# Kernel tuning notes

Hardware: AMD Instinct MI355X
Metric: run time of the kernel (lower is better)

## Reference

```python
import jax, jax.numpy as jnp
import numpy as np

NUM_CLASSES = 6

def _weight_matrix(num_classes, weight_type='quadratic'):
    i = jnp.arange(num_classes, dtype=jnp.float32)
    d = jnp.abs(i[:, None] - i[None, :])
    if weight_type == 'linear':
        return d
    elif weight_type == 'quadratic':
        return d ** 2
    else:
        raise ValueError("weight_type must be 'linear' or 'quadratic'")

def setup_inputs() -> dict:
    key = jax.random.key(0)
    k1, k2 = jax.random.split(key)
    N = 4_000_000
    y_pred = jax.random.normal(k1, (N, NUM_CLASSES), dtype=jnp.float32)
    y_true = jax.random.randint(k2, (N,), 0, NUM_CLASSES, dtype=jnp.int64)
    return {"y_pred": y_pred, "y_true": y_true}

def reference(y_pred, y_true):
    C = NUM_CLASSES
    t = y_true.reshape(-1).astype(jnp.int32)
    probs = jax.nn.softmax(y_pred, axis=1)
    p = jnp.argmax(probs, axis=1).astype(jnp.int32)
    # histograms over classes (equivalent to torch.histc with bins=C, min=0, max=C-1)
    hist_true = jnp.bincount(t, length=C).astype(jnp.float32)
    hist_pred = jnp.bincount(p, length=C).astype(jnp.float32)
    # confusion matrix in one fused scatter-add pass (replaces the Python loop)
    flat = t * C + p  # [N]
    confusion = jnp.bincount(flat, length=C * C).astype(jnp.float32).reshape(C, C)
    confusion = confusion / confusion.sum()
    expected = jnp.outer(hist_true, hist_pred)
    expected = expected / expected.sum()
    W = _weight_matrix(C, 'quadratic')
    kappa = 1.0 - (W * confusion).sum() / (W * expected).sum()
    return kappa
```

## Files before the change

kernel.cpp:

```cpp
#include <hip/hip_runtime.h>


#define NC 6
#define NBINS 36
#define GRID 1024
#define SEGS 16
#define FIN_THREADS (NBINS * SEGS)

__global__ void kappa_count_kernel(const float4* __restrict__ yp4,
                                   const int2* __restrict__ yt2,
                                   const float* __restrict__ yp,
                                   const int* __restrict__ yt,
                                   unsigned int* __restrict__ gconf,
                                   int npairs, int N) {
    __shared__ unsigned int sconf[NBINS];
    const int tid = threadIdx.x;
    if (tid < NBINS) sconf[tid] = 0u;
    __syncthreads();

    const int stride = gridDim.x * blockDim.x;
    for (int i = blockIdx.x * blockDim.x + tid; i < npairs; i += stride) {
        const float4 a = yp4[3 * i];
        const float4 b = yp4[3 * i + 1];
        const float4 c = yp4[3 * i + 2];
        const int2 t = yt2[i];

        float m = a.x; int p = 0;
        if (a.y > m) { m = a.y; p = 1; }
        if (a.z > m) { m = a.z; p = 2; }
        if (a.w > m) { m = a.w; p = 3; }
        if (b.x > m) { m = b.x; p = 4; }
        if (b.y > m) { m = b.y; p = 5; }
        atomicAdd(&sconf[t.x * NC + p], 1u);

        m = b.z; p = 0;
        if (b.w > m) { m = b.w; p = 1; }
        if (c.x > m) { m = c.x; p = 2; }
        if (c.y > m) { m = c.y; p = 3; }
        if (c.z > m) { m = c.z; p = 4; }
        if (c.w > m) { m = c.w; p = 5; }
        atomicAdd(&sconf[t.y * NC + p], 1u);
    }

    if ((N & 1) && blockIdx.x == 0 && tid == 0) {
        const int r = N - 1;
        float m = yp[r * NC]; int p = 0;
        #pragma unroll
        for (int j = 1; j < NC; ++j) {
            const float v = yp[r * NC + j];
            if (v > m) { m = v; p = j; }
        }
        atomicAdd(&sconf[yt[r] * NC + p], 1u);
    }

    __syncthreads();
    if (tid < NBINS) gconf[blockIdx.x * NBINS + tid] = sconf[tid];
}

__global__ void kappa_final_kernel(const unsigned int* __restrict__ gconf,
                                   float* __restrict__ out, long long N) {
    __shared__ unsigned int part[SEGS][NBINS];
    __shared__ unsigned int conf_s[NBINS];
    const int tid = threadIdx.x;
    if (tid < FIN_THREADS) {
        const int bin = tid % NBINS;
        const int seg = tid / NBINS;
        unsigned int s = 0;
        const int b0 = seg * (GRID / SEGS);
        #pragma unroll 8
        for (int b = b0; b < b0 + GRID / SEGS; ++b) s += gconf[b * NBINS + bin];
        part[seg][bin] = s;
    }
    __syncthreads();
    if (tid < NBINS) {
        unsigned int tot = 0;
        #pragma unroll
        for (int s2 = 0; s2 < SEGS; ++s2) tot += part[s2][tid];
        conf_s[tid] = tot;
    }
    __syncthreads();
    if (tid == 0) {
        long long conf[NBINS], ht[NC], hp[NC];
        #pragma unroll
        for (int i = 0; i < NC; ++i) { ht[i] = 0; hp[i] = 0; }
        #pragma unroll
        for (int k = 0; k < NBINS; ++k) conf[k] = (long long)conf_s[k];

        long long num = 0;
        #pragma unroll
        for (int i = 0; i < NC; ++i)
            #pragma unroll
            for (int j = 0; j < NC; ++j) {
                const long long w = (long long)(i - j) * (i - j);
                num += w * conf[i * NC + j];
                ht[i] += conf[i * NC + j];
                hp[j] += conf[i * NC + j];
            }
        long long den = 0;
        #pragma unroll
        for (int i = 0; i < NC; ++i)
            #pragma unroll
            for (int j = 0; j < NC; ++j)
                den += (long long)(i - j) * (i - j) * ht[i] * hp[j];

        out[0] = (float)(1.0 - ((double)num * (double)N) / (double)den);
    }
}

extern "C" void kernel_launch(void* const* d_in, const int* in_sizes, int n_in,
                              void* d_out, int out_size, void* d_ws, size_t ws_size,
                              hipStream_t stream) {
    const float* yp = (const float*)d_in[0];
    const int* yt = (const int*)d_in[1];
    const int N = in_sizes[1];
    unsigned int* gconf = (unsigned int*)d_ws;

    const int npairs = N / 2;
    kappa_count_kernel<<<GRID, 256, 0, stream>>>(
        (const float4*)yp, (const int2*)yt, yp, yt, gconf, npairs, N);
    kappa_final_kernel<<<1, FIN_THREADS, 0, stream>>>(gconf, (float*)d_out,
                                                      (long long)N);
}
```

Baseline: 153.3 us.

## Fuse count and finalize kernels via last-block atomic reduction with replicated bins

Merges the counting and final reduction kernels into one launch: each block adds its 36 bins into one of 8 replicated global bin sets with atomics, and the last block, found through an atomic counter, sums the replicas and computes kappa. Shared histograms are split into 4 copies, one per 64-thread wavefront, to reduce LDS atomic contention. The grid is doubled to 2048 blocks. This removes the second launch and the 1024-row partial-sum pass, at the cost of a memset per call and global atomic traffic.

Measured after the change: 244.4 us. 1.59x slower.

```diff
diff --git a/kernel.cpp b/kernel.cpp
--- a/kernel.cpp
+++ b/kernel.cpp
@@ -3,21 +3,25 @@
 
 #define NC 6
 #define NBINS 36
-#define GRID 1024
-#define SEGS 16
-#define FIN_THREADS (NBINS * SEGS)
+#define NREP 8
+#define GRID 2048
+#define BLOCK 256
 
-__global__ void kappa_count_kernel(const float4* __restrict__ yp4,
-                                   const int2* __restrict__ yt2,
-                                   const float* __restrict__ yp,
-                                   const int* __restrict__ yt,
-                                   unsigned int* __restrict__ gconf,
-                                   int npairs, int N) {
-    __shared__ unsigned int sconf[NBINS];
+__global__ __launch_bounds__(BLOCK) void kappa_fused(
+    const float4* __restrict__ yp4, const int2* __restrict__ yt2,
+    const float* __restrict__ yp, const int* __restrict__ yt,
+    unsigned int* __restrict__ gbins,
+    unsigned int* __restrict__ counter,
+    float* __restrict__ out, int npairs, int N) {
+    __shared__ unsigned int sconf[4][NBINS];
+    __shared__ unsigned int stot[NBINS];
+    __shared__ unsigned int last_flag;
     const int tid = threadIdx.x;
-    if (tid < NBINS) sconf[tid] = 0u;
+    if (tid < 4 * NBINS) ((unsigned int*)sconf)[tid] = 0u;
+    if (tid == 0) last_flag = 0u;
     __syncthreads();
 
+    unsigned int* __restrict__ my = sconf[tid >> 6];
     const int stride = gridDim.x * blockDim.x;
     for (int i = blockIdx.x * blockDim.x + tid; i < npairs; i += stride) {
         const float4 a = yp4[3 * i];
@@ -31,7 +35,7 @@
         if (a.w > m) { m = a.w; p = 3; }
         if (b.x > m) { m = b.x; p = 4; }
         if (b.y > m) { m = b.y; p = 5; }
-        atomicAdd(&sconf[t.x * NC + p], 1u);
+        atomicAdd(&my[t.x * NC + p], 1u);
 
         m = b.z; p = 0;
         if (b.w > m) { m = b.w; p = 1; }
@@ -39,7 +43,7 @@
         if (c.y > m) { m = c.y; p = 3; }
         if (c.z > m) { m = c.z; p = 4; }
         if (c.w > m) { m = c.w; p = 5; }
-        atomicAdd(&sconf[t.y * NC + p], 1u);
+        atomicAdd(&my[t.y * NC + p], 1u);
     }
 
     if ((N & 1) && blockIdx.x == 0 && tid == 0) {
@@ -50,33 +54,31 @@
             const float v = yp[r * NC + j];
             if (v > m) { m = v; p = j; }
         }
-        atomicAdd(&sconf[yt[r] * NC + p], 1u);
-    }
-
-    __syncthreads();
-    if (tid < NBINS) gconf[blockIdx.x * NBINS + tid] = sconf[tid];
-}
-
-__global__ void kappa_final_kernel(const unsigned int* __restrict__ gconf,
-                                   float* __restrict__ out, long long N) {
-    __shared__ unsigned int part[SEGS][NBINS];
-    __shared__ unsigned int conf_s[NBINS];
-    const int tid = threadIdx.x;
-    if (tid < FIN_THREADS) {
-        const int bin = tid % NBINS;
-        const int seg = tid / NBINS;
-        unsigned int s = 0;
-        const int b0 = seg * (GRID / SEGS);
-        #pragma unroll 8
-        for (int b = b0; b < b0 + GRID / SEGS; ++b) s += gconf[b * NBINS + bin];
-        part[seg][bin] = s;
+        atomicAdd(&my[yt[r] * NC + p], 1u);
     }
     __syncthreads();
+
     if (tid < NBINS) {
-        unsigned int tot = 0;
+        const unsigned int s =
+            sconf[0][tid] + sconf[1][tid] + sconf[2][tid] + sconf[3][tid];
+        if (s) atomicAdd(&gbins[(blockIdx.x & (NREP - 1)) * NBINS + tid], s);
+    }
+    __syncthreads();
+
+    if (tid == 0) {
+        __threadfence();
+        if (atomicAdd(counter, 1u) == (unsigned int)(GRID - 1)) last_flag = 1u;
+    }
+    __syncthreads();
+    if (!last_flag) return;
+
+    if (tid < NBINS) {
+        unsigned int s = 0;
         #pragma unroll
-        for (int s2 = 0; s2 < SEGS; ++s2) tot += part[s2][tid];
-        conf_s[tid] = tot;
+        for (int r = 0; r < NREP; ++r)
+            s += __hip_atomic_load(&gbins[r * NBINS + tid], __ATOMIC_RELAXED,
+                                   __HIP_MEMORY_SCOPE_AGENT);
+        stot[tid] = s;
     }
     __syncthreads();
     if (tid == 0) {
@@ -84,7 +86,7 @@
         #pragma unroll
         for (int i = 0; i < NC; ++i) { ht[i] = 0; hp[i] = 0; }
         #pragma unroll
-        for (int k = 0; k < NBINS; ++k) conf[k] = (long long)conf_s[k];
+        for (int k = 0; k < NBINS; ++k) conf[k] = (long long)stot[k];
 
         long long num = 0;
         #pragma unroll
@@ -103,7 +105,7 @@
             for (int j = 0; j < NC; ++j)
                 den += (long long)(i - j) * (i - j) * ht[i] * hp[j];
 
-        out[0] = (float)(1.0 - ((double)num * (double)N) / (double)den);
+        out[0] = (float)(1.0 - ((double)num * (double)(long long)N) / (double)den);
     }
 }
 
@@ -113,11 +115,13 @@
     const float* yp = (const float*)d_in[0];
     const int* yt = (const int*)d_in[1];
     const int N = in_sizes[1];
-    unsigned int* gconf = (unsigned int*)d_ws;
+    unsigned int* gbins = (unsigned int*)d_ws;
+    unsigned int* counter = gbins + NREP * NBINS;
+
+    hipMemsetAsync(d_ws, 0, (NREP * NBINS + 1) * sizeof(unsigned int), stream);
 
     const int npairs = N / 2;
-    kappa_count_kernel<<<GRID, 256, 0, stream>>>(
-        (const float4*)yp, (const int2*)yt, yp, yt, gconf, npairs, N);
-    kappa_final_kernel<<<1, FIN_THREADS, 0, stream>>>(gconf, (float*)d_out,
-                                                      (long long)N);
+    kappa_fused<<<GRID, BLOCK, 0, stream>>>(
+        (const float4*)yp, (const int2*)yt, yp, yt, gbins, counter,
+        (float*)d_out, npairs, N);
 }
```

## Stage loads through LDS per wave and privatize histograms per wave

Applied to the files above, without the earlier changes.

Each wave now loads a 64-pair chunk of predictions with contiguous, coalesced float4 reads into shared memory, then reads back each lane's 6-float rows. The confusion histogram is privatized per wave in shared memory and summed at block end, so fewer threads contend on the same 36 LDS atomic counters. The launch changes to 512 blocks of 1024 threads, and a tail path handles pairs left over after the last full chunk. It relies on wave-level lockstep with only a block fence between the LDS write and read, and it uses more shared memory per block.

Measured after the change: 155.6 us. About the same (+1.5%).

```diff
diff --git a/kernel.cpp b/kernel.cpp
--- a/kernel.cpp
+++ b/kernel.cpp
@@ -3,27 +3,42 @@
 
 #define NC 6
 #define NBINS 36
-#define GRID 1024
+#define BLOCK 1024
+#define NWAVES (BLOCK / 64)
+#define GRID 512
+#define CHUNK 64
 #define SEGS 16
 #define FIN_THREADS (NBINS * SEGS)
 
-__global__ void kappa_count_kernel(const float4* __restrict__ yp4,
-                                   const int2* __restrict__ yt2,
-                                   const float* __restrict__ yp,
-                                   const int* __restrict__ yt,
-                                   unsigned int* __restrict__ gconf,
-                                   int npairs, int N) {
-    __shared__ unsigned int sconf[NBINS];
+__global__ __launch_bounds__(BLOCK, 8) void kappa_count(
+    const float4* __restrict__ yp4, const int2* __restrict__ yt2,
+    const float* __restrict__ yp, const int* __restrict__ yt,
+    unsigned int* __restrict__ gconf, int npairs, int N) {
+    __shared__ float4 stage[NWAVES][3 * CHUNK];
+    __shared__ unsigned int sconf[NWAVES][NBINS];
     const int tid = threadIdx.x;
-    if (tid < NBINS) sconf[tid] = 0u;
+    const int w = tid >> 6;
+    const int L = tid & 63;
+    if (tid < NWAVES * NBINS) ((unsigned int*)sconf)[tid] = 0u;
     __syncthreads();
 
-    const int stride = gridDim.x * blockDim.x;
-    for (int i = blockIdx.x * blockDim.x + tid; i < npairs; i += stride) {
-        const float4 a = yp4[3 * i];
-        const float4 b = yp4[3 * i + 1];
-        const float4 c = yp4[3 * i + 2];
-        const int2 t = yt2[i];
+    unsigned int* my = sconf[w];
+    float4* st = stage[w];
+
+    const int nchunks = npairs / CHUNK;
+    const int gwaves = GRID * NWAVES;
+    for (int c = blockIdx.x * NWAVES + w; c < nchunks; c += gwaves) {
+        const float4 g0 = yp4[c * 3 * CHUNK + L];
+        const float4 g1 = yp4[c * 3 * CHUNK + 64 + L];
+        const float4 g2 = yp4[c * 3 * CHUNK + 128 + L];
+        const int2 t = yt2[c * CHUNK + L];
+        st[L] = g0;
+        st[64 + L] = g1;
+        st[128 + L] = g2;
+        __threadfence_block();
+        const float4 a = st[3 * L];
+        const float4 b = st[3 * L + 1];
+        const float4 d = st[3 * L + 2];
 
         float m = a.x; int p = 0;
         if (a.y > m) { m = a.y; p = 1; }
@@ -31,15 +46,38 @@
         if (a.w > m) { m = a.w; p = 3; }
         if (b.x > m) { m = b.x; p = 4; }
         if (b.y > m) { m = b.y; p = 5; }
-        atomicAdd(&sconf[t.x * NC + p], 1u);
+        atomicAdd(&my[t.x * NC + p], 1u);
 
         m = b.z; p = 0;
         if (b.w > m) { m = b.w; p = 1; }
-        if (c.x > m) { m = c.x; p = 2; }
-        if (c.y > m) { m = c.y; p = 3; }
-        if (c.z > m) { m = c.z; p = 4; }
-        if (c.w > m) { m = c.w; p = 5; }
-        atomicAdd(&sconf[t.y * NC + p], 1u);
+        if (d.x > m) { m = d.x; p = 2; }
+        if (d.y > m) { m = d.y; p = 3; }
+        if (d.z > m) { m = d.z; p = 4; }
+        if (d.w > m) { m = d.w; p = 5; }
+        atomicAdd(&my[t.y * NC + p], 1u);
+    }
+
+    const int rem0 = nchunks * CHUNK;
+    if (blockIdx.x == 0 && tid < npairs - rem0) {
+        const int i = rem0 + tid;
+        const float4 a = yp4[3 * i];
+        const float4 b = yp4[3 * i + 1];
+        const float4 d = yp4[3 * i + 2];
+        const int2 t = yt2[i];
+        float m = a.x; int p = 0;
+        if (a.y > m) { m = a.y; p = 1; }
+        if (a.z > m) { m = a.z; p = 2; }
+        if (a.w > m) { m = a.w; p = 3; }
+        if (b.x > m) { m = b.x; p = 4; }
+        if (b.y > m) { m = b.y; p = 5; }
+        atomicAdd(&my[t.x * NC + p], 1u);
+        m = b.z; p = 0;
+        if (b.w > m) { m = b.w; p = 1; }
+        if (d.x > m) { m = d.x; p = 2; }
+        if (d.y > m) { m = d.y; p = 3; }
+        if (d.z > m) { m = d.z; p = 4; }
+        if (d.w > m) { m = d.w; p = 5; }
+        atomicAdd(&my[t.y * NC + p], 1u);
     }
 
     if ((N & 1) && blockIdx.x == 0 && tid == 0) {
@@ -50,11 +88,16 @@
             const float v = yp[r * NC + j];
             if (v > m) { m = v; p = j; }
         }
-        atomicAdd(&sconf[yt[r] * NC + p], 1u);
+        atomicAdd(&my[yt[r] * NC + p], 1u);
     }
 
     __syncthreads();
-    if (tid < NBINS) gconf[blockIdx.x * NBINS + tid] = sconf[tid];
+    if (tid < NBINS) {
+        unsigned int s = 0;
+        #pragma unroll
+        for (int k = 0; k < NWAVES; ++k) s += sconf[k][tid];
+        gconf[blockIdx.x * NBINS + tid] = s;
+    }
 }
 
 __global__ void kappa_final_kernel(const unsigned int* __restrict__ gconf,
@@ -116,7 +159,7 @@
     unsigned int* gconf = (unsigned int*)d_ws;
 
     const int npairs = N / 2;
-    kappa_count_kernel<<<GRID, 256, 0, stream>>>(
+    kappa_count<<<GRID, BLOCK, 0, stream>>>(
         (const float4*)yp, (const int2*)yt, yp, yt, gconf, npairs, N);
     kappa_final_kernel<<<1, FIN_THREADS, 0, stream>>>(gconf, (float*)d_out,
                                                       (long long)N);
```
